# Performance work log

Hardware: AMD Instinct MI355X
Metric: run time of the kernel (lower is better)

The kernel has to match this reference:

```python
import jax, jax.numpy as jnp
import numpy as np
import math

K = 10  # k_neighbors (k = min(10, N-1) = 10 since N=2048)


def setup_inputs() -> dict:
    key = jax.random.key(0)
    k1, k2, k3, k4 = jax.random.split(key, 4)
    N, T, H = 2048, 512, 256
    E_fixed = 65536
    x = jax.random.normal(k1, (N, T, H), dtype=jnp.float32)
    fixed_edge_index = jax.random.randint(k2, (2, E_fixed), 0, N, dtype=jnp.int64)
    fixed_edge_attr = jax.random.uniform(k3, (E_fixed, 1), dtype=jnp.float32)
    W = jax.random.normal(k4, (H // 2, H), dtype=jnp.float32) / math.sqrt(H)
    mix_alpha = 0.3
    mix_logit = jnp.array([math.log(mix_alpha / (1.0 - mix_alpha + 1e-08))], dtype=jnp.float32)
    return {"x": x, "fixed_edge_index": fixed_edge_index,
            "fixed_edge_attr": fixed_edge_attr, "W": W, "mix_logit": mix_logit}


def reference(x, fixed_edge_index, fixed_edge_attr, W, mix_logit):
    # x: [N, T, H]; W: [H//2, H]; mix_logit: [1]
    N = x.shape[0]
    x_agg = x.mean(axis=1)                                  # [N, H] temporal mean-pool
    e = x_agg @ W.T                                         # [N, H//2] bias-free projection
    e = e / jnp.maximum(jnp.linalg.norm(e, axis=-1, keepdims=True), 1e-12)  # F.normalize
    sim = e @ e.T                                           # [N, N] cosine similarity
    topk_vals, topk_idx = jax.lax.top_k(sim, K + 1)         # self-sim (=1) is in column 0
    topk_vals = topk_vals[:, 1:]                            # [N, K] drop self-loop
    topk_idx = topk_idx[:, 1:]
    src = jnp.repeat(jnp.arange(N, dtype=fixed_edge_index.dtype), K)  # [N*K]
    dst = topk_idx.reshape(-1).astype(fixed_edge_index.dtype)
    dyn_edge_index = jnp.stack([src, dst], axis=0)          # [2, N*K]
    dyn_edge_attr = topk_vals.reshape(-1, 1)                # [N*K, 1]
    alpha = jax.nn.sigmoid(mix_logit[0])
    combined_edge_index = jnp.concatenate([fixed_edge_index, dyn_edge_index], axis=1)
    combined_edge_attr = jnp.concatenate(
        [fixed_edge_attr * (1.0 - alpha), dyn_edge_attr * alpha], axis=0)
    return combined_edge_index, combined_edge_attr
```

## Files before the change

kernel.cpp:

```cpp
#include <hip/hip_runtime.h>
#include <hip/hip_bf16.h>
#include <math.h>


__global__ __launch_bounds__(256) void mean_kernel(const float* __restrict__ x,
                                                   float* __restrict__ xagg,
                                                   int T, int H) {
    const int n   = blockIdx.x;
    const int tid = threadIdx.x;
    const int v   = tid & 63;
    const int tg  = tid >> 6;

    const float4* xr = reinterpret_cast<const float4*>(x + (size_t)n * T * H);
    float4 acc = make_float4(0.f, 0.f, 0.f, 0.f);
    for (int t = tg; t < T; t += 4) {
        float4 d = xr[t * 64 + v];
        acc.x += d.x; acc.y += d.y; acc.z += d.z; acc.w += d.w;
    }
    __shared__ float4 red[256];
    red[tid] = acc;
    __syncthreads();
    if (tid < 64) {
        float4 a = red[tid], b = red[tid + 64], c = red[tid + 128], d = red[tid + 192];
        float s = 1.0f / (float)T;
        float4 o;
        o.x = (a.x + b.x + c.x + d.x) * s;
        o.y = (a.y + b.y + c.y + d.y) * s;
        o.z = (a.z + b.z + c.z + d.z) * s;
        o.w = (a.w + b.w + c.w + d.w) * s;
        reinterpret_cast<float4*>(xagg + (size_t)n * H)[v] = o;
    }
}

__global__ __launch_bounds__(128) void proj_norm_kernel(const float* __restrict__ xagg,
                                                        const float* __restrict__ W,
                                                        float* __restrict__ e,
                                                        int H ) {
    const int n = blockIdx.x;
    const int j = threadIdx.x;

    __shared__ float xs[256];
    xs[j]       = xagg[(size_t)n * H + j];
    xs[j + 128] = xagg[(size_t)n * H + j + 128];
    __syncthreads();

    const float* Wr = W + (size_t)j * H;
    float acc = 0.f;
    #pragma unroll 8
    for (int c = 0; c < 256; ++c) acc = fmaf(Wr[c], xs[c], acc);

    float s = acc * acc;
    #pragma unroll
    for (int off = 32; off; off >>= 1) s += __shfl_xor(s, off);
    __shared__ float nrm[2];
    if ((j & 63) == 0) nrm[j >> 6] = s;
    __syncthreads();
    float tot = nrm[0] + nrm[1];
    float inv = 1.0f / fmaxf(sqrtf(tot), 1e-12f);
    e[(size_t)n * 128 + j] = acc * inv;
}

#define TK_ROWS 4
__global__ __launch_bounds__(256) void simtopk_kernel(const float* __restrict__ e,
                                                      const float* __restrict__ mix,
                                                      float* __restrict__ out,
                                                      int N , int E ) {
    __shared__ float eL[TK_ROWS][128];
    __shared__ float simL[TK_ROWS][2048];

    const int i0  = blockIdx.x * TK_ROWS;
    const int tid = threadIdx.x;
    const int M   = E + N * 10;

    {
        int r = tid >> 6;
        int c = tid & 63;
        const float* er = e + (size_t)(i0 + r) * 128;
        eL[r][c]      = er[c];
        eL[r][c + 64] = er[c + 64];
    }
    __syncthreads();

    for (int j = tid; j < N; j += 256) {
        const float4* ej = reinterpret_cast<const float4*>(e + (size_t)j * 128);
        float acc[TK_ROWS] = {0.f, 0.f, 0.f, 0.f};
        #pragma unroll 4
        for (int c4 = 0; c4 < 32; ++c4) {
            float4 vv = ej[c4];
            #pragma unroll
            for (int r = 0; r < TK_ROWS; ++r) {
                const float* el = &eL[r][c4 * 4];
                acc[r] = fmaf(vv.x, el[0], acc[r]);
                acc[r] = fmaf(vv.y, el[1], acc[r]);
                acc[r] = fmaf(vv.z, el[2], acc[r]);
                acc[r] = fmaf(vv.w, el[3], acc[r]);
            }
        }
        #pragma unroll
        for (int r = 0; r < TK_ROWS; ++r) simL[r][j] = acc[r];
    }
    __syncthreads();

    const int w    = tid >> 6;
    const int lane = tid & 63;
    const int i    = i0 + w;
    const float alpha = 1.0f / (1.0f + expf(-mix[0]));

    float keepv = 0.f;
    int   keepi = 0;
    for (int round = 0; round < 11; ++round) {
        float bv = -3.0f;
        int   bi = N;
        for (int t = 0; t < 32; ++t) {
            int j = t * 64 + lane;
            float v = simL[w][j];
            if (v > bv || (v == bv && j < bi)) { bv = v; bi = j; }
        }
        #pragma unroll
        for (int off = 32; off; off >>= 1) {
            float ov = __shfl_xor(bv, off);
            int   oi = __shfl_xor(bi, off);
            if (ov > bv || (ov == bv && oi < bi)) { bv = ov; bi = oi; }
        }
        if ((bi & 63) == lane && bi < N) simL[w][bi] = -3.0f;
        if (lane == round) { keepv = bv; keepi = bi; }
    }
    if (lane >= 1 && lane <= 10) {
        int kk  = lane - 1;
        int pos = i * 10 + kk;
        out[(size_t)E + pos]               = (float)i;
        out[(size_t)M + E + pos]           = (float)keepi;
        out[2 * (size_t)M + E + pos]       = keepv * alpha;
    }
}

__global__ __launch_bounds__(256) void fixed_kernel(const int* __restrict__ ei,
                                                    const float* __restrict__ ea,
                                                    const float* __restrict__ mix,
                                                    float* __restrict__ out,
                                                    int E, int M) {
    const int idx = blockIdx.x * blockDim.x + threadIdx.x;
    if (idx < E) {
        float alpha = 1.0f / (1.0f + expf(-mix[0]));
        out[idx]                    = (float)ei[idx];
        out[(size_t)M + idx]        = (float)ei[E + idx];
        out[2 * (size_t)M + idx]    = ea[idx] * (1.0f - alpha);
    }
}

extern "C" void kernel_launch(void* const* d_in, const int* in_sizes, int n_in,
                              void* d_out, int out_size, void* d_ws, size_t ws_size,
                              hipStream_t stream) {
    const float* x   = (const float*)d_in[0];
    const int*   ei  = (const int*)d_in[1];
    const float* ea  = (const float*)d_in[2];
    const float* W   = (const float*)d_in[3];
    const float* mix = (const float*)d_in[4];

    const int H  = 256;
    const int E  = in_sizes[2];
    const int M  = out_size / 3;
    const int N  = (M - E) / 10;
    const int T  = (int)((size_t)in_sizes[0] / ((size_t)N * H));

    float* xagg = (float*)d_ws;
    float* e    = xagg + (size_t)N * H;
    float* out  = (float*)d_out;

    mean_kernel<<<N, 256, 0, stream>>>(x, xagg, T, H);
    proj_norm_kernel<<<N, 128, 0, stream>>>(xagg, W, e, H);
    simtopk_kernel<<<N / TK_ROWS, 256, 0, stream>>>(e, mix, out, N, E);
    fixed_kernel<<<(E + 255) / 256, 256, 0, stream>>>(ei, ea, mix, out, E, M);
}
```

Baseline: 307.0 us.

## Use nontemporal contiguous mean loads and register-tile the similarity loop

The mean kernel now has each wave sum a contiguous quarter of the timesteps, using nontemporal vector loads and an unrolled loop, so the 2 GB streaming read bypasses cache retention. The similarity kernel, when N is 2048, keeps 8 columns per thread in registers and loads the four query vectors from shared memory once per chunk instead of once per column. This cuts LDS traffic and adds memory-level parallelism, at the cost of more registers and a specialised code path. The mean pass is bandwidth-bound and dominates the total time, so the gain depends mostly on the load change.

```diff
diff --git a/kernel.cpp b/kernel.cpp
--- a/kernel.cpp
+++ b/kernel.cpp
@@ -1,6 +1,8 @@
 #include <hip/hip_runtime.h>
 #include <hip/hip_bf16.h>
 #include <math.h>
+
+typedef float f4 __attribute__((ext_vector_type(4)));
 
 
 __global__ __launch_bounds__(256) void mean_kernel(const float* __restrict__ x,
@@ -10,25 +12,24 @@
     const int tid = threadIdx.x;
     const int v   = tid & 63;
     const int tg  = tid >> 6;
-
-    const float4* xr = reinterpret_cast<const float4*>(x + (size_t)n * T * H);
-    float4 acc = make_float4(0.f, 0.f, 0.f, 0.f);
-    for (int t = tg; t < T; t += 4) {
-        float4 d = xr[t * 64 + v];
-        acc.x += d.x; acc.y += d.y; acc.z += d.z; acc.w += d.w;
-    }
-    __shared__ float4 red[256];
+    const int TQ  = T >> 2;
+
+    const f4* xr = reinterpret_cast<const f4*>(x + (size_t)n * T * H)
+                 + (size_t)tg * TQ * 64;
+    f4 acc = {0.f, 0.f, 0.f, 0.f};
+    #pragma unroll 4
+    for (int t = 0; t < TQ; ++t) {
+        f4 d = __builtin_nontemporal_load(&xr[t * 64 + v]);
+        acc += d;
+    }
+    __shared__ f4 red[256];
     red[tid] = acc;
     __syncthreads();
     if (tid < 64) {
-        float4 a = red[tid], b = red[tid + 64], c = red[tid + 128], d = red[tid + 192];
+        f4 o = (red[tid] + red[tid + 64]) + (red[tid + 128] + red[tid + 192]);
         float s = 1.0f / (float)T;
-        float4 o;
-        o.x = (a.x + b.x + c.x + d.x) * s;
-        o.y = (a.y + b.y + c.y + d.y) * s;
-        o.z = (a.z + b.z + c.z + d.z) * s;
-        o.w = (a.w + b.w + c.w + d.w) * s;
-        reinterpret_cast<float4*>(xagg + (size_t)n * H)[v] = o;
+        o *= s;
+        reinterpret_cast<f4*>(xagg + (size_t)n * H)[v] = o;
     }
 }
 
@@ -81,23 +82,53 @@
     }
     __syncthreads();
 
-    for (int j = tid; j < N; j += 256) {
-        const float4* ej = reinterpret_cast<const float4*>(e + (size_t)j * 128);
-        float acc[TK_ROWS] = {0.f, 0.f, 0.f, 0.f};
-        #pragma unroll 4
+    if (N == 2048) {
+        float acc[TK_ROWS][8];
+        #pragma unroll
+        for (int r = 0; r < TK_ROWS; ++r)
+            #pragma unroll
+            for (int q = 0; q < 8; ++q) acc[r][q] = 0.f;
+
         for (int c4 = 0; c4 < 32; ++c4) {
-            float4 vv = ej[c4];
-            #pragma unroll
-            for (int r = 0; r < TK_ROWS; ++r) {
-                const float* el = &eL[r][c4 * 4];
-                acc[r] = fmaf(vv.x, el[0], acc[r]);
-                acc[r] = fmaf(vv.y, el[1], acc[r]);
-                acc[r] = fmaf(vv.z, el[2], acc[r]);
-                acc[r] = fmaf(vv.w, el[3], acc[r]);
+            f4 qv[TK_ROWS];
+            #pragma unroll
+            for (int r = 0; r < TK_ROWS; ++r)
+                qv[r] = *reinterpret_cast<const f4*>(&eL[r][c4 * 4]);
+            #pragma unroll
+            for (int q = 0; q < 8; ++q) {
+                f4 vj = *reinterpret_cast<const f4*>(e + (size_t)(q * 256 + tid) * 128 + c4 * 4);
+                #pragma unroll
+                for (int r = 0; r < TK_ROWS; ++r) {
+                    acc[r][q] = fmaf(vj.x, qv[r].x, acc[r][q]);
+                    acc[r][q] = fmaf(vj.y, qv[r].y, acc[r][q]);
+                    acc[r][q] = fmaf(vj.z, qv[r].z, acc[r][q]);
+                    acc[r][q] = fmaf(vj.w, qv[r].w, acc[r][q]);
+                }
             }
         }
         #pragma unroll
-        for (int r = 0; r < TK_ROWS; ++r) simL[r][j] = acc[r];
+        for (int r = 0; r < TK_ROWS; ++r)
+            #pragma unroll
+            for (int q = 0; q < 8; ++q)
+                simL[r][q * 256 + tid] = acc[r][q];
+    } else {
+        for (int j = tid; j < N; j += 256) {
+            const f4* ej = reinterpret_cast<const f4*>(e + (size_t)j * 128);
+            float acc[TK_ROWS] = {0.f, 0.f, 0.f, 0.f};
+            for (int c4 = 0; c4 < 32; ++c4) {
+                f4 vv = ej[c4];
+                #pragma unroll
+                for (int r = 0; r < TK_ROWS; ++r) {
+                    const float* el = &eL[r][c4 * 4];
+                    acc[r] = fmaf(vv.x, el[0], acc[r]);
+                    acc[r] = fmaf(vv.y, el[1], acc[r]);
+                    acc[r] = fmaf(vv.z, el[2], acc[r]);
+                    acc[r] = fmaf(vv.w, el[3], acc[r]);
+                }
+            }
+            #pragma unroll
+            for (int r = 0; r < TK_ROWS; ++r) simL[r][j] = acc[r];
+        }
     }
     __syncthreads();
 
@@ -128,9 +159,9 @@
     if (lane >= 1 && lane <= 10) {
         int kk  = lane - 1;
         int pos = i * 10 + kk;
-        out[(size_t)E + pos]               = (float)i;
-        out[(size_t)M + E + pos]           = (float)keepi;
-        out[2 * (size_t)M + E + pos]       = keepv * alpha;
+        out[(size_t)E + pos]         = (float)i;
+        out[(size_t)M + E + pos]     = (float)keepi;
+        out[2 * (size_t)M + E + pos] = keepv * alpha;
     }
 }
 
@@ -142,9 +173,9 @@
     const int idx = blockIdx.x * blockDim.x + threadIdx.x;
     if (idx < E) {
         float alpha = 1.0f / (1.0f + expf(-mix[0]));
-        out[idx]                    = (float)ei[idx];
-        out[(size_t)M + idx]        = (float)ei[E + idx];
-        out[2 * (size_t)M + idx]    = ea[idx] * (1.0f - alpha);
+        out[idx]                 = (float)ei[idx];
+        out[(size_t)M + idx]     = (float)ei[E + idx];
+        out[2 * (size_t)M + idx] = ea[idx] * (1.0f - alpha);
     }
 }
 
```

Measured after the change: 389.6 us. 26.9% more time.
